# Performance work log

Hardware: AMD Instinct MI355X
Metric: run time of the kernel (lower is better)

Reference implementation:

```python
import jax, jax.numpy as jnp
import numpy as np

KEY_DIM = 32
NUM_HEADS = 8
ATTN_RATIO = 2
D = ATTN_RATIO * KEY_DIM          # 64, per-head value dim
DH = D * NUM_HEADS                # 512
NH_KD = KEY_DIM * NUM_HEADS       # 256
H_QKV = DH + 2 * NH_KD            # 1024
DIM = 512
IMG = 1024                        # img_shape (32x32)
S = 32                            # sqrt(IMG)
ATT = 1044                        # att_shape = N
B = 16
EPS = 1e-5


def hardswish(x):
    return x * jnp.clip(x + 3.0, 0.0, 6.0) / 6.0


def setup_inputs() -> dict:
    key = jax.random.key(0)
    ks = jax.random.split(key, 8)
    x = jax.random.normal(ks[0], (B, ATT, DIM), dtype=jnp.float32)
    qkv_w = jax.random.normal(ks[1], (H_QKV, DIM), dtype=jnp.float32) * 0.02
    bn_gamma = jnp.ones((H_QKV,), dtype=jnp.float32)
    bn_beta = jnp.zeros((H_QKV,), dtype=jnp.float32)
    bn_mean = jax.random.normal(ks[2], (H_QKV,), dtype=jnp.float32) * 0.01
    bn_var = jax.random.uniform(ks[3], (H_QKV,), minval=0.5, maxval=1.5, dtype=jnp.float32)
    conv_w = jax.random.normal(ks[4], (DH, 1, 3, 3), dtype=jnp.float32) * 0.1  # depthwise
    conv_b = jnp.zeros((DH,), dtype=jnp.float32)
    proj_w = jax.random.normal(ks[5], (IMG, ATT), dtype=jnp.float32) * 0.02
    proj_b = jnp.zeros((IMG,), dtype=jnp.float32)
    out_w = jax.random.normal(ks[6], (DIM, DH), dtype=jnp.float32) * 0.02
    out_b = jnp.zeros((DIM,), dtype=jnp.float32)
    return {"x": x, "qkv_w": qkv_w, "bn_gamma": bn_gamma, "bn_beta": bn_beta,
            "bn_mean": bn_mean, "bn_var": bn_var, "conv_w": conv_w, "conv_b": conv_b,
            "proj_w": proj_w, "proj_b": proj_b, "out_w": out_w, "out_b": out_b}


def reference(x, qkv_w, bn_gamma, bn_beta, bn_mean, bn_var,
              conv_w, conv_b, proj_w, proj_b, out_w, out_b):
    Bb, N, C = x.shape
    # Linear_BN: linear (no bias) + BatchNorm1d (eval, running stats)
    qkv = jnp.einsum('bnc,hc->bnh', x, qkv_w)
    qkv = (qkv - bn_mean) * (bn_gamma * jax.lax.rsqrt(bn_var + EPS)) + bn_beta
    qkv = qkv.reshape(Bb, N, NUM_HEADS, 2 * KEY_DIM + D)
    q = qkv[..., :KEY_DIM].transpose(0, 2, 1, 3)                 # (B,H,N,kd)
    k = qkv[..., KEY_DIM:2 * KEY_DIM].transpose(0, 2, 1, 3)      # (B,H,N,kd)
    v = qkv[..., 2 * KEY_DIM:].transpose(0, 2, 1, 3)             # (B,H,N,d)
    # parallel depthwise conv branch: raw reshape (B,H,IMG,d) -> (B,DH,S,S), as in torch
    v0 = v[:, :, :IMG, :].reshape(Bb, DH, S, S)
    vc = jax.lax.conv_general_dilated(
        hardswish(v0), conv_w, window_strides=(1, 1), padding='SAME',
        dimension_numbers=('NCHW', 'OIHW', 'NCHW'), feature_group_count=DH)
    vc = (vc + conv_b[None, :, None, None]).reshape(Bb, DH, IMG)  # (B,DH,IMG)
    # attention
    attn = jax.nn.softmax(jnp.einsum('bhnk,bhmk->bhnm', q, k) * (KEY_DIM ** -0.5), axis=-1)
    o = jnp.einsum('bhnm,bhmd->bhnd', attn, v)                   # (B,H,N,d)
    # torch: (attn@v).transpose(1,2).reshape(B,-1,N) -> raw flatten of (B,N,H,d) into (B,DH,N)
    o = o.transpose(0, 2, 1, 3).reshape(Bb, DH, N)
    xo = jnp.einsum('bdn,mn->bdm', o, proj_w) + proj_b + vc       # (B,DH,IMG)
    out = jnp.einsum('bmd,cd->bmc', xo.transpose(0, 2, 1), out_w) + out_b  # (B,IMG,DIM)
    return out
```

## Files before the change

kernel.cpp:

```cpp
#include <hip/hip_runtime.h>
#include <hip/hip_fp16.h>

typedef _Float16 f16;
typedef _Float16 f16x8 __attribute__((ext_vector_type(8)));
typedef _Float16 f16x4 __attribute__((ext_vector_type(4)));
typedef float    f32x4 __attribute__((ext_vector_type(4)));
typedef float    f32x16 __attribute__((ext_vector_type(16)));

#define DEV __device__ __forceinline__

DEV int imin(int a, int b) { return a < b ? a : b; }

#if defined(__has_builtin)
#  if __has_builtin(__builtin_amdgcn_exp2f)
#    define EXP2(x) __builtin_amdgcn_exp2f(x)
#  else
#    define EXP2(x) __expf((x) * 0.6931471805599453f)
#  endif
#else
#  define EXP2(x) __expf((x) * 0.6931471805599453f)
#endif

#define QSCALE (0.17677669529663687f * 1.4426950408889634f)


constexpr size_t OFF_XH   = 0;
constexpr size_t OFF_WQ   = 17104896;
constexpr size_t OFF_PW   = 18153472;
constexpr size_t OFF_OW   = 20316160;
constexpr size_t OFF_BNA  = 20840448;
constexpr size_t OFF_BNB  = 20844544;
constexpr size_t OFF_QB   = 20848640;
constexpr size_t OFF_KB   = 30285824;
constexpr size_t OFF_VT   = 39198720;
constexpr size_t OFF_OPAD = 57024512;
constexpr size_t OFF_VCT  = 74326016;
constexpr size_t OFF_XOT  = 91103232;

DEV f32x16 zero16() {
  f32x16 z;
  #pragma unroll
  for (int i = 0; i < 16; ++i) z[i] = 0.f;
  return z;
}

DEV unsigned pk2(float a, float b) {
  auto h = __builtin_amdgcn_cvt_pkrtz(a, b);
  union { decltype(h) x; unsigned u; } t;
  t.x = h;
  return t.u;
}

DEV void plswap(unsigned &a, unsigned &b) {
  asm("v_permlane32_swap_b32 %0, %1" : "+v"(a), "+v"(b));
}

union W4 { unsigned w[4]; f16x8 v; };

DEV void pack_block(const float p[16], f16x8 &a0, f16x8 &a1) {
  unsigned w0 = pk2(p[0], p[1]),   w1 = pk2(p[2], p[3]);
  unsigned w2 = pk2(p[4], p[5]),   w3 = pk2(p[6], p[7]);
  unsigned w4 = pk2(p[8], p[9]),   w5 = pk2(p[10], p[11]);
  unsigned w6 = pk2(p[12], p[13]), w7 = pk2(p[14], p[15]);
  plswap(w0, w2); plswap(w1, w3);
  plswap(w4, w6); plswap(w5, w7);
  W4 u; u.w[0] = w0; u.w[1] = w1; u.w[2] = w2; u.w[3] = w3; a0 = u.v;
  W4 v; v.w[0] = w4; v.w[1] = w5; v.w[2] = w6; v.w[3] = w7; a1 = v.v;
}

__global__ __launch_bounds__(256) void prep_kernel(
    const float* __restrict__ x, const float* __restrict__ qkv_w,
    const float* __restrict__ bn_g, const float* __restrict__ bn_b,
    const float* __restrict__ bn_m, const float* __restrict__ bn_v,
    const float* __restrict__ proj_w, const float* __restrict__ out_w,
    f16* __restrict__ x_h, f16* __restrict__ wq_h, f16* __restrict__ pw_h,
    f16* __restrict__ ow_h, float* __restrict__ bn_a, float* __restrict__ bn_sh,
    f16* __restrict__ qb, f16* __restrict__ kb, f16* __restrict__ vt,
    f16* __restrict__ opad)
{
  long tid = (long)blockIdx.x * blockDim.x + threadIdx.x;
  long gsz = (long)gridDim.x * blockDim.x;

  for (long i = tid; i < 2138112; i += gsz) {
    float4 f = ((const float4*)x)[i];
    f16x4 o = {(f16)f.x, (f16)f.y, (f16)f.z, (f16)f.w};
    ((f16x4*)x_h)[i] = o;
  }
  for (long i = tid; i < 524288; i += gsz) wq_h[i] = (f16)qkv_w[i];
  for (long i = tid; i < 1081344; i += gsz) {
    long m = i / 1056, nn = i - m * 1056;
    pw_h[i] = (nn < 1044) ? (f16)proj_w[m * 1044 + nn] : (f16)0.f;
  }
  for (long i = tid; i < 262144; i += gsz) ow_h[i] = (f16)out_w[i];
  for (long i = tid; i < 1024; i += gsz) {
    float a = bn_g[i] * rsqrtf(bn_v[i] + 1e-5f);
    bn_a[i] = a;
    bn_sh[i] = bn_b[i] - bn_m[i] * a;
  }
  for (long i = tid; i < 13824; i += gsz) {
    int bh = (int)(i / 108);
    int nn = 1044 + (int)(i - (long)bh * 108);
    f16* q = qb + ((long)bh * 1152 + nn) * 32;
    for (int j = 0; j < 32; ++j) q[j] = (f16)0.f;
  }
  for (long i = tid; i < 5632; i += gsz) {
    int bh = (int)(i / 44);
    int nn = 1044 + (int)(i - (long)bh * 44);
    f16* k = kb + ((long)bh * 1088 + nn) * 32;
    for (int j = 0; j < 32; ++j) k[j] = (f16)0.f;
  }
  for (long i = tid; i < 8192; i += gsz) {
    f16* v = vt + i * 1088 + 1044;
    for (int j = 0; j < 44; ++j) v[j] = (f16)0.f;
  }
  for (long i = tid; i < 8192; i += gsz) {
    f16* o = opad + i * 1056 + 1044;
    for (int j = 0; j < 12; ++j) o[j] = (f16)0.f;
  }
}

DEV void gemm_core(const f16* __restrict__ A, const f16* __restrict__ B,
                   int lda, int ldb, int kIters, int rowClampA, int rowClampB,
                   f16* As, f16* Bs, f32x4 acc[4][4])
{
  const int t = threadIdx.x;
  const int wave = t >> 6, lane = t & 63;
  const int wr = wave >> 1, wc = wave & 1;
  const int r0 = t >> 2, seg = t & 3;
  const int fr = lane & 15, fg = lane >> 4;
  const int ra0 = imin(r0, rowClampA);
  const int ra1 = imin(r0 + 64, rowClampA);
  const int rb0 = imin(r0, rowClampB);
  const int rb1 = imin(r0 + 64, rowClampB);

  const f16* pa0 = A + (long)ra0 * lda + seg * 8;
  const f16* pa1 = A + (long)ra1 * lda + seg * 8;
  const f16* pb0 = B + (long)rb0 * ldb + seg * 8;
  const f16* pb1 = B + (long)rb1 * ldb + seg * 8;

  f16x8 a0, a1, b0, b1;
  a0 = *(const f16x8*)(pa0);
  a1 = *(const f16x8*)(pa1);
  b0 = *(const f16x8*)(pb0);
  b1 = *(const f16x8*)(pb1);

  #pragma unroll 1
  for (int kt = 0; kt < kIters; ++kt) {
    __syncthreads();
    *(f16x8*)(As + r0 * 40 + seg * 8) = a0;
    *(f16x8*)(As + (r0 + 64) * 40 + seg * 8) = a1;
    *(f16x8*)(Bs + r0 * 40 + seg * 8) = b0;
    *(f16x8*)(Bs + (r0 + 64) * 40 + seg * 8) = b1;
    __syncthreads();
    if (kt + 1 < kIters) {
      const int kb = (kt + 1) * 32;
      a0 = *(const f16x8*)(pa0 + kb);
      a1 = *(const f16x8*)(pa1 + kb);
      b0 = *(const f16x8*)(pb0 + kb);
      b1 = *(const f16x8*)(pb1 + kb);
    }
    f16x8 af[4], bf[4];
    #pragma unroll
    for (int m = 0; m < 4; ++m)
      af[m] = *(const f16x8*)(As + (wr * 64 + m * 16 + fr) * 40 + fg * 8);
    #pragma unroll
    for (int n = 0; n < 4; ++n)
      bf[n] = *(const f16x8*)(Bs + (wc * 64 + n * 16 + fr) * 40 + fg * 8);
    #pragma unroll
    for (int m = 0; m < 4; ++m)
      #pragma unroll
      for (int n = 0; n < 4; ++n)
        acc[m][n] = __builtin_amdgcn_mfma_f32_16x16x32_f16(af[m], bf[n], acc[m][n], 0, 0, 0);
  }
}

__global__ __launch_bounds__(256) void qkv_gemm(
    const f16* __restrict__ x_h, const f16* __restrict__ wq,
    const float* __restrict__ bn_a, const float* __restrict__ bn_sh,
    f16* __restrict__ qb, f16* __restrict__ kb, f16* __restrict__ vt)
{
  __shared__ f16 As[128 * 40];
  __shared__ f16 Bs[128 * 40];
  const int id = blockIdx.x + blockIdx.y * 8;
  const int lin = (id & 7) * 131 + (id >> 3);
  const int row0 = (lin & 7) * 128;
  const int col0 = (lin >> 3) * 128;
  f32x4 acc[4][4];
  #pragma unroll
  for (int m = 0; m < 4; ++m)
    #pragma unroll
    for (int n = 0; n < 4; ++n) acc[m][n] = (f32x4){0.f, 0.f, 0.f, 0.f};
  gemm_core(wq + (long)row0 * 512, x_h + (long)col0 * 512, 512, 512, 16,
            1 << 30, 16703 - col0, As, Bs, acc);
  const int lane = threadIdx.x & 63, wave = threadIdx.x >> 6;
  const int wr = wave >> 1, wc = wave & 1, fr = lane & 15, fg = lane >> 4;
  #pragma unroll
  for (int m = 0; m < 4; ++m) {
    const int chBase = row0 + wr * 64 + m * 16 + fg * 4;
    const float4 ba4 = *(const float4*)(bn_a + chBase);
    const float4 bs4 = *(const float4*)(bn_sh + chBase);
    const int hh = chBase >> 7, r = chBase & 127;
    #pragma unroll
    for (int n = 0; n < 4; ++n) {
      int tok = col0 + wc * 64 + n * 16 + fr;
      if (tok < 16704) {
        int bi = tok / 1044;
        int ni = tok - bi * 1044;
        long bh = (long)(bi * 8 + hh);
        float v0 = acc[m][n][0] * ba4.x + bs4.x;
        float v1 = acc[m][n][1] * ba4.y + bs4.y;
        float v2 = acc[m][n][2] * ba4.z + bs4.z;
        float v3 = acc[m][n][3] * ba4.w + bs4.w;
        if (r < 32) {
          f16x4 pk = {(f16)(v0 * QSCALE), (f16)(v1 * QSCALE),
                      (f16)(v2 * QSCALE), (f16)(v3 * QSCALE)};
          *(f16x4*)(qb + (bh * 1152 + ni) * 32 + r) = pk;
        } else if (r < 64) {
          f16x4 pk = {(f16)v0, (f16)v1, (f16)v2, (f16)v3};
          *(f16x4*)(kb + (bh * 1088 + ni) * 32 + (r - 32)) = pk;
        } else {
          f16* vp = vt + (bh * 64 + (r - 64)) * 1088 + ni;
          vp[0]        = (f16)v0;
          vp[1088]     = (f16)v1;
          vp[2 * 1088] = (f16)v2;
          vp[3 * 1088] = (f16)v3;
        }
      }
    }
  }
}

__global__ __launch_bounds__(256) void conv_kernel(
    const f16* __restrict__ vt, const float* __restrict__ conv_w,
    const float* __restrict__ conv_b, f16* __restrict__ vcT)
{
  __shared__ f16 img[16][34][36];
  const int b = blockIdx.y, g = blockIdx.x;
  const int c0 = g * 16, h = c0 >> 6, ci0 = c0 & 63;
  const int t = threadIdx.x;
  for (int i = t; i < 16 * 34 * 36; i += 256) ((f16*)img)[i] = (f16)0.f;
  __syncthreads();
  const int d = t >> 2, seg = t & 3;
  const f16* src = vt + ((long)(b * 8 + h) * 64 + d) * 1088 + ci0 * 16 + seg * 64;
  const int dhib = d >> 5;
  const int s2 = d & 31;
  #pragma unroll
  for (int j = 0; j < 8; ++j) {
    f16x8 vv = *(const f16x8*)(src + j * 8);
    #pragma unroll
    for (int e = 0; e < 8; ++e) {
      int local = seg * 64 + j * 8 + e;
      int cl = local >> 4, rr = local & 15;
      float xv = (float)vv[e];
      float hs = xv * fminf(fmaxf(xv + 3.f, 0.f), 6.f) * (1.f / 6.f);
      img[cl][1 + rr * 2 + dhib][1 + s2] = (f16)hs;
    }
  }
  __syncthreads();
  const int cl = t & 15, pg = t >> 4;
  const int c = c0 + cl;
  float w[9];
  #pragma unroll
  for (int i = 0; i < 9; ++i) w[i] = conv_w[c * 9 + i];
  const float bias = conv_b[c];
  for (int i = 0; i < 64; ++i) {
    int p = pg + i * 16;
    int s1 = p >> 5, ss2 = p & 31;
    float a = bias;
    #pragma unroll
    for (int di = 0; di < 3; ++di)
      #pragma unroll
      for (int dj = 0; dj < 3; ++dj)
        a += w[di * 3 + dj] * (float)img[cl][s1 + di][ss2 + dj];
    vcT[((long)b * 1024 + p) * 512 + c] = (f16)a;
  }
}

__global__ __launch_bounds__(256, 4) void attn_kernel(
    const f16* __restrict__ qb, const f16* __restrict__ kb,
    const f16* __restrict__ vt, f16* __restrict__ opad)
{
  __shared__ f16 kls[2][4 * 32 * 8];
  __shared__ f16 vls[2][4 * 64 * 8];
  __shared__ float l_sh[4][32];

  const int id = blockIdx.x + blockIdx.y * 9;
  const int xcd = id & 7, sl = id >> 3;
  const int bh = xcd * 16 + sl / 9, qblk = sl % 9;
  const int b = bh >> 3, h = bh & 7;
  const int t = threadIdx.x;
  const int wave = t >> 6, lane = t & 63;
  const int lq = lane & 31, hi = lane >> 5;
  const int q0 = qblk * 128 + wave * 32;

  const f16* qb_ = qb + (long)bh * 1152 * 32;
  const f16* kb_ = kb + (long)bh * 1088 * 32;
  const f16* vt_ = vt + (long)bh * 64 * 1088;

  const f16x8 qf0 = *(const f16x8*)(qb_ + (long)(q0 + lq) * 32 + hi * 8);
  const f16x8 qf1 = *(const f16x8*)(qb_ + (long)(q0 + lq) * 32 + 16 + hi * 8);

  const int sk_k = t >> 3, sk_s8 = t & 7;
  const int sk_seg = sk_s8 >> 1, sk_half = sk_s8 & 1;
  const int sv_d = t >> 2, sv_p = t & 3;
  const int wkoff = (sk_seg * 32 + ((sk_k + sk_seg) & 31)) * 16 + sk_half * 8;
  const int wvoff = (sv_p * 64 + ((sv_d + sv_p) & 63)) * 16;
  int koff[2], voff[2][2];
  #pragma unroll
  for (int ss = 0; ss < 2; ++ss) {
    int ss2 = 2 * ss + hi;
    koff[ss] = (ss2 * 32 + ((lq + ss2) & 31)) * 16;
  }
  #pragma unroll
  for (int nd = 0; nd < 2; ++nd)
    #pragma unroll
    for (int ks = 0; ks < 2; ++ks) {
      int kk4 = 2 * ks + hi;
      voff[nd][ks] = (kk4 * 64 + ((nd * 32 + lq + kk4) & 63)) * 16;
    }

  f16x4 stk;
  f16x8 stv;
  auto load_tile = [&](int kt) {
    stk = *(const f16x4*)(kb_ + (long)(kt * 32 + sk_k) * 32 + sk_s8 * 4);
    stv = *(const f16x8*)(vt_ + (long)sv_d * 1088 + kt * 32 + sv_p * 8);
  };
  auto write_tile = [&](int buf) {
    *(f16x4*)((char*)kls[buf] + wkoff) = stk;
    *(f16x8*)((char*)vls[buf] + wvoff) = stv;
  };

  f32x16 o0 = zero16(), o1 = zero16();
  float lsum = 0.f;

  load_tile(0);
  write_tile(0);
  __syncthreads();

  int cur = 0;
  #pragma unroll 1
  for (int kt = 0; kt < 33; ++kt) {
    if (kt < 32) load_tile(kt + 1);
    const char* kcur = (const char*)kls[cur];
    const char* vcur = (const char*)vls[cur];
    f16x8 kf0 = *(const f16x8*)(kcur + koff[0]);
    f16x8 kf1 = *(const f16x8*)(kcur + koff[1]);
    f32x16 s = zero16();
    s = __builtin_amdgcn_mfma_f32_32x32x16_f16(kf0, qf0, s, 0, 0, 0);
    s = __builtin_amdgcn_mfma_f32_32x32x16_f16(kf1, qf1, s, 0, 0, 0);
    float p[16];
    #pragma unroll
    for (int r = 0; r < 16; ++r) p[r] = EXP2(s[r]);
    if (kt == 32) {
      #pragma unroll
      for (int r = 0; r < 16; ++r) {
        int cr = (r & 3) + 8 * (r >> 2) + 4 * hi;
        p[r] = (cr < 20) ? p[r] : 0.f;
      }
    }
    float t8[8];
    #pragma unroll
    for (int r = 0; r < 8; ++r) t8[r] = p[r] + p[r + 8];
    lsum += ((t8[0] + t8[1]) + (t8[2] + t8[3])) + ((t8[4] + t8[5]) + (t8[6] + t8[7]));
    f16x8 pa0, pa1;
    pack_block(p, pa0, pa1);
    __builtin_amdgcn_s_setprio(1);
    {
      f16x8 vf00 = *(const f16x8*)(vcur + voff[0][0]);
      f16x8 vf10 = *(const f16x8*)(vcur + voff[1][0]);
      o0 = __builtin_amdgcn_mfma_f32_32x32x16_f16(pa0, vf00, o0, 0, 0, 0);
      o1 = __builtin_amdgcn_mfma_f32_32x32x16_f16(pa0, vf10, o1, 0, 0, 0);
      f16x8 vf01 = *(const f16x8*)(vcur + voff[0][1]);
      f16x8 vf11 = *(const f16x8*)(vcur + voff[1][1]);
      o0 = __builtin_amdgcn_mfma_f32_32x32x16_f16(pa1, vf01, o0, 0, 0, 0);
      o1 = __builtin_amdgcn_mfma_f32_32x32x16_f16(pa1, vf11, o1, 0, 0, 0);
    }
    __builtin_amdgcn_s_setprio(0);
    if (kt < 32) write_tile(cur ^ 1);
    __syncthreads();
    cur ^= 1;
  }

  lsum += __shfl_xor(lsum, 32);
  l_sh[wave][lq] = lsum;
  __syncthreads();
  float invl[16];
  #pragma unroll
  for (int r = 0; r < 16; ++r) {
    int cr = (r & 3) + 8 * (r >> 2) + 4 * hi;
    invl[r] = __builtin_amdgcn_rcpf(l_sh[wave][cr]);
  }
  #pragma unroll
  for (int nd = 0; nd < 2; ++nd) {
    #pragma unroll
    for (int r = 0; r < 16; ++r) {
      int cr = (r & 3) + 8 * (r >> 2) + 4 * hi;
      int q = q0 + cr;
      if (q < 1044) {
        float val = (nd ? o1[r] : o0[r]) * invl[r];
        unsigned flat = (unsigned)q * 512u + (unsigned)h * 64u + (unsigned)(nd * 32 + lq);
        unsigned c = flat / 1044u;
        unsigned np = flat - c * 1044u;
        opad[((long)b * 512 + c) * 1056 + np] = (f16)val;
      }
    }
  }
}

__global__ __launch_bounds__(256) void proj_gemm(
    const f16* __restrict__ pw, const f16* __restrict__ opad,
    const float* __restrict__ proj_b, const f16* __restrict__ vcT,
    f16* __restrict__ xoT)
{
  __shared__ f16 As[128 * 40];
  __shared__ f16 Bs[128 * 40];
  const int id = blockIdx.x + blockIdx.y * 4 + blockIdx.z * 32;
  const int lin = (id & 7) * 64 + (id >> 3);
  const int b = lin >> 5;
  const int rc = lin & 31;
  const int row0 = (rc >> 2) * 128;
  const int col0 = (rc & 3) * 128;
  f32x4 acc[4][4];
  #pragma unroll
  for (int m = 0; m < 4; ++m)
    #pragma unroll
    for (int n = 0; n < 4; ++n) acc[m][n] = (f32x4){0.f, 0.f, 0.f, 0.f};
  gemm_core(pw + (long)row0 * 1056, opad + ((long)b * 512 + col0) * 1056,
            1056, 1056, 33, 1 << 30, 1 << 30, As, Bs, acc);
  const int lane = threadIdx.x & 63, wave = threadIdx.x >> 6;
  const int wr = wave >> 1, wc = wave & 1, fr = lane & 15, fg = lane >> 4;
  #pragma unroll
  for (int m = 0; m < 4; ++m) {
    #pragma unroll
    for (int rr = 0; rr < 4; ++rr) {
      int mi = row0 + wr * 64 + m * 16 + fg * 4 + rr;
      float pb = proj_b[mi];
      #pragma unroll
      for (int n = 0; n < 4; ++n) {
        int c = col0 + wc * 64 + n * 16 + fr;
        long idx = ((long)b * 1024 + mi) * 512 + c;
        xoT[idx] = (f16)(acc[m][n][rr] + pb + (float)vcT[idx]);
      }
    }
  }
}

__global__ __launch_bounds__(256) void out_gemm(
    const f16* __restrict__ xoT, const f16* __restrict__ ow,
    const float* __restrict__ out_b, float* __restrict__ out)
{
  __shared__ f16 As[128 * 40];
  __shared__ f16 Bs[128 * 40];
  const int id = blockIdx.x + blockIdx.y * 4 + blockIdx.z * 32;
  const int lin = (id & 7) * 64 + (id >> 3);
  const int b = lin >> 5;
  const int rc = lin & 31;
  const int row0 = (rc >> 2) * 128;
  const int col0 = (rc & 3) * 128;
  f32x4 acc[4][4];
  #pragma unroll
  for (int m = 0; m < 4; ++m)
    #pragma unroll
    for (int n = 0; n < 4; ++n) acc[m][n] = (f32x4){0.f, 0.f, 0.f, 0.f};
  gemm_core(xoT + ((long)b * 1024 + row0) * 512, ow + (long)col0 * 512,
            512, 512, 16, 1 << 30, 1 << 30, As, Bs, acc);
  const int lane = threadIdx.x & 63, wave = threadIdx.x >> 6;
  const int wr = wave >> 1, wc = wave & 1, fr = lane & 15, fg = lane >> 4;
  float ob[4];
  #pragma unroll
  for (int n = 0; n < 4; ++n) ob[n] = out_b[col0 + wc * 64 + n * 16 + fr];
  #pragma unroll
  for (int m = 0; m < 4; ++m) {
    #pragma unroll
    for (int rr = 0; rr < 4; ++rr) {
      int mi = row0 + wr * 64 + m * 16 + fg * 4 + rr;
      #pragma unroll
      for (int n = 0; n < 4; ++n) {
        int co = col0 + wc * 64 + n * 16 + fr;
        out[((long)b * 1024 + mi) * 512 + co] = acc[m][n][rr] + ob[n];
      }
    }
  }
}

extern "C" void kernel_launch(void* const* d_in, const int* in_sizes, int n_in,
                              void* d_out, int out_size, void* d_ws, size_t ws_size,
                              hipStream_t stream) {
  const float* x      = (const float*)d_in[0];
  const float* qkv_w  = (const float*)d_in[1];
  const float* bn_g   = (const float*)d_in[2];
  const float* bn_b   = (const float*)d_in[3];
  const float* bn_m   = (const float*)d_in[4];
  const float* bn_v   = (const float*)d_in[5];
  const float* conv_w = (const float*)d_in[6];
  const float* conv_b = (const float*)d_in[7];
  const float* proj_w = (const float*)d_in[8];
  const float* proj_b = (const float*)d_in[9];
  const float* out_w  = (const float*)d_in[10];
  const float* out_b  = (const float*)d_in[11];
  float* out = (float*)d_out;

  char* ws = (char*)d_ws;
  f16*   x_h   = (f16*)(ws + OFF_XH);
  f16*   wq_h  = (f16*)(ws + OFF_WQ);
  f16*   pw_h  = (f16*)(ws + OFF_PW);
  f16*   ow_h  = (f16*)(ws + OFF_OW);
  float* bn_a  = (float*)(ws + OFF_BNA);
  float* bn_sh = (float*)(ws + OFF_BNB);
  f16*   qb    = (f16*)(ws + OFF_QB);
  f16*   kb    = (f16*)(ws + OFF_KB);
  f16*   vt    = (f16*)(ws + OFF_VT);
  f16*   opad  = (f16*)(ws + OFF_OPAD);
  f16*   vcT   = (f16*)(ws + OFF_VCT);
  f16*   xoT   = (f16*)(ws + OFF_XOT);

  prep_kernel<<<1024, 256, 0, stream>>>(x, qkv_w, bn_g, bn_b, bn_m, bn_v,
                                        proj_w, out_w, x_h, wq_h, pw_h, ow_h,
                                        bn_a, bn_sh, qb, kb, vt, opad);
  qkv_gemm<<<dim3(8, 131), 256, 0, stream>>>(x_h, wq_h, bn_a, bn_sh, qb, kb, vt);
  conv_kernel<<<dim3(32, 16), 256, 0, stream>>>(vt, conv_w, conv_b, vcT);
  attn_kernel<<<dim3(9, 128), 256, 0, stream>>>(qb, kb, vt, opad);
  proj_gemm<<<dim3(4, 8, 16), 256, 0, stream>>>(pw_h, opad, proj_b, vcT, xoT);
  out_gemm<<<dim3(4, 8, 16), 256, 0, stream>>>(xoT, ow_h, out_b, out);
}
```

Baseline: 176.0 us.

## Have each attention wave process two 32-row query tiles to reuse K/V fragments

Halves the attention block size to two waves, and each wave now handles 64 query rows as two 32-row sub-tiles sharing the same K and V fragments loaded from LDS. Staging loads are widened so 128 threads still fill the K/V tiles, and the final normalisation reads per-row sums for both sub-tiles. This cuts LDS reads and barrier overhead per unit of MFMA work, at the cost of doubled accumulator registers and fewer waves per block, which may lower occupancy.

```diff
diff --git a/kernel.cpp b/kernel.cpp
--- a/kernel.cpp
+++ b/kernel.cpp
@@ -276,13 +276,13 @@
   }
 }
 
-__global__ __launch_bounds__(256, 4) void attn_kernel(
+__global__ __launch_bounds__(128) void attn_kernel(
     const f16* __restrict__ qb, const f16* __restrict__ kb,
     const f16* __restrict__ vt, f16* __restrict__ opad)
 {
   __shared__ f16 kls[2][4 * 32 * 8];
   __shared__ f16 vls[2][4 * 64 * 8];
-  __shared__ float l_sh[4][32];
+  __shared__ float l_sh[2][64];
 
   const int id = blockIdx.x + blockIdx.y * 9;
   const int xcd = id & 7, sl = id >> 3;
@@ -291,20 +291,23 @@
   const int t = threadIdx.x;
   const int wave = t >> 6, lane = t & 63;
   const int lq = lane & 31, hi = lane >> 5;
-  const int q0 = qblk * 128 + wave * 32;
+  const int q0 = qblk * 128 + wave * 64;
 
   const f16* qb_ = qb + (long)bh * 1152 * 32;
   const f16* kb_ = kb + (long)bh * 1088 * 32;
   const f16* vt_ = vt + (long)bh * 64 * 1088;
 
-  const f16x8 qf0 = *(const f16x8*)(qb_ + (long)(q0 + lq) * 32 + hi * 8);
-  const f16x8 qf1 = *(const f16x8*)(qb_ + (long)(q0 + lq) * 32 + 16 + hi * 8);
-
-  const int sk_k = t >> 3, sk_s8 = t & 7;
-  const int sk_seg = sk_s8 >> 1, sk_half = sk_s8 & 1;
-  const int sv_d = t >> 2, sv_p = t & 3;
-  const int wkoff = (sk_seg * 32 + ((sk_k + sk_seg) & 31)) * 16 + sk_half * 8;
-  const int wvoff = (sv_p * 64 + ((sv_d + sv_p) & 63)) * 16;
+  const f16x8 qfA0 = *(const f16x8*)(qb_ + (long)(q0 + lq) * 32 + hi * 8);
+  const f16x8 qfA1 = *(const f16x8*)(qb_ + (long)(q0 + lq) * 32 + 16 + hi * 8);
+  const f16x8 qfB0 = *(const f16x8*)(qb_ + (long)(q0 + 32 + lq) * 32 + hi * 8);
+  const f16x8 qfB1 = *(const f16x8*)(qb_ + (long)(q0 + 32 + lq) * 32 + 16 + hi * 8);
+
+  const int sk_k = t >> 2, sk_s = t & 3;
+  const int sv_d = t >> 1, sv_p = t & 1;
+  const int c0v = 2 * sv_p, c1v = c0v + 1;
+  const int wkoff = (sk_s * 32 + ((sk_k + sk_s) & 31)) * 16;
+  const int wvoff0 = (c0v * 64 + ((sv_d + c0v) & 63)) * 16;
+  const int wvoff1 = (c1v * 64 + ((sv_d + c1v) & 63)) * 16;
   int koff[2], voff[2][2];
   #pragma unroll
   for (int ss = 0; ss < 2; ++ss) {
@@ -319,19 +322,20 @@
       voff[nd][ks] = (kk4 * 64 + ((nd * 32 + lq + kk4) & 63)) * 16;
     }
 
-  f16x4 stk;
-  f16x8 stv;
+  f16x8 stk, stv0, stv1;
   auto load_tile = [&](int kt) {
-    stk = *(const f16x4*)(kb_ + (long)(kt * 32 + sk_k) * 32 + sk_s8 * 4);
-    stv = *(const f16x8*)(vt_ + (long)sv_d * 1088 + kt * 32 + sv_p * 8);
+    stk  = *(const f16x8*)(kb_ + (long)(kt * 32 + sk_k) * 32 + sk_s * 8);
+    stv0 = *(const f16x8*)(vt_ + (long)sv_d * 1088 + kt * 32 + sv_p * 16);
+    stv1 = *(const f16x8*)(vt_ + (long)sv_d * 1088 + kt * 32 + sv_p * 16 + 8);
   };
   auto write_tile = [&](int buf) {
-    *(f16x4*)((char*)kls[buf] + wkoff) = stk;
-    *(f16x8*)((char*)vls[buf] + wvoff) = stv;
+    *(f16x8*)((char*)kls[buf] + wkoff)  = stk;
+    *(f16x8*)((char*)vls[buf] + wvoff0) = stv0;
+    *(f16x8*)((char*)vls[buf] + wvoff1) = stv1;
   };
 
-  f32x16 o0 = zero16(), o1 = zero16();
-  float lsum = 0.f;
+  f32x16 oA0 = zero16(), oA1 = zero16(), oB0 = zero16(), oB1 = zero16();
+  float lsumA = 0.f, lsumB = 0.f;
 
   load_tile(0);
   write_tile(0);
@@ -345,35 +349,46 @@
     const char* vcur = (const char*)vls[cur];
     f16x8 kf0 = *(const f16x8*)(kcur + koff[0]);
     f16x8 kf1 = *(const f16x8*)(kcur + koff[1]);
-    f32x16 s = zero16();
-    s = __builtin_amdgcn_mfma_f32_32x32x16_f16(kf0, qf0, s, 0, 0, 0);
-    s = __builtin_amdgcn_mfma_f32_32x32x16_f16(kf1, qf1, s, 0, 0, 0);
-    float p[16];
-    #pragma unroll
-    for (int r = 0; r < 16; ++r) p[r] = EXP2(s[r]);
+    f32x16 sA = zero16(), sB = zero16();
+    sA = __builtin_amdgcn_mfma_f32_32x32x16_f16(kf0, qfA0, sA, 0, 0, 0);
+    sB = __builtin_amdgcn_mfma_f32_32x32x16_f16(kf0, qfB0, sB, 0, 0, 0);
+    sA = __builtin_amdgcn_mfma_f32_32x32x16_f16(kf1, qfA1, sA, 0, 0, 0);
+    sB = __builtin_amdgcn_mfma_f32_32x32x16_f16(kf1, qfB1, sB, 0, 0, 0);
+    float pA[16], pB[16];
+    #pragma unroll
+    for (int r = 0; r < 16; ++r) { pA[r] = EXP2(sA[r]); pB[r] = EXP2(sB[r]); }
     if (kt == 32) {
       #pragma unroll
       for (int r = 0; r < 16; ++r) {
         int cr = (r & 3) + 8 * (r >> 2) + 4 * hi;
-        p[r] = (cr < 20) ? p[r] : 0.f;
+        pA[r] = (cr < 20) ? pA[r] : 0.f;
+        pB[r] = (cr < 20) ? pB[r] : 0.f;
       }
     }
     float t8[8];
     #pragma unroll
-    for (int r = 0; r < 8; ++r) t8[r] = p[r] + p[r + 8];
-    lsum += ((t8[0] + t8[1]) + (t8[2] + t8[3])) + ((t8[4] + t8[5]) + (t8[6] + t8[7]));
-    f16x8 pa0, pa1;
-    pack_block(p, pa0, pa1);
+    for (int r = 0; r < 8; ++r) t8[r] = pA[r] + pA[r + 8];
+    lsumA += ((t8[0] + t8[1]) + (t8[2] + t8[3])) + ((t8[4] + t8[5]) + (t8[6] + t8[7]));
+    #pragma unroll
+    for (int r = 0; r < 8; ++r) t8[r] = pB[r] + pB[r + 8];
+    lsumB += ((t8[0] + t8[1]) + (t8[2] + t8[3])) + ((t8[4] + t8[5]) + (t8[6] + t8[7]));
+    f16x8 paA0, paA1, paB0, paB1;
+    pack_block(pA, paA0, paA1);
+    pack_block(pB, paB0, paB1);
     __builtin_amdgcn_s_setprio(1);
     {
       f16x8 vf00 = *(const f16x8*)(vcur + voff[0][0]);
       f16x8 vf10 = *(const f16x8*)(vcur + voff[1][0]);
-      o0 = __builtin_amdgcn_mfma_f32_32x32x16_f16(pa0, vf00, o0, 0, 0, 0);
-      o1 = __builtin_amdgcn_mfma_f32_32x32x16_f16(pa0, vf10, o1, 0, 0, 0);
+      oA0 = __builtin_amdgcn_mfma_f32_32x32x16_f16(paA0, vf00, oA0, 0, 0, 0);
+      oB0 = __builtin_amdgcn_mfma_f32_32x32x16_f16(paB0, vf00, oB0, 0, 0, 0);
+      oA1 = __builtin_amdgcn_mfma_f32_32x32x16_f16(paA0, vf10, oA1, 0, 0, 0);
+      oB1 = __builtin_amdgcn_mfma_f32_32x32x16_f16(paB0, vf10, oB1, 0, 0, 0);
       f16x8 vf01 = *(const f16x8*)(vcur + voff[0][1]);
       f16x8 vf11 = *(const f16x8*)(vcur + voff[1][1]);
-      o0 = __builtin_amdgcn_mfma_f32_32x32x16_f16(pa1, vf01, o0, 0, 0, 0);
-      o1 = __builtin_amdgcn_mfma_f32_32x32x16_f16(pa1, vf11, o1, 0, 0, 0);
+      oA0 = __builtin_amdgcn_mfma_f32_32x32x16_f16(paA1, vf01, oA0, 0, 0, 0);
+      oB0 = __builtin_amdgcn_mfma_f32_32x32x16_f16(paB1, vf01, oB0, 0, 0, 0);
+      oA1 = __builtin_amdgcn_mfma_f32_32x32x16_f16(paA1, vf11, oA1, 0, 0, 0);
+      oB1 = __builtin_amdgcn_mfma_f32_32x32x16_f16(paB1, vf11, oB1, 0, 0, 0);
     }
     __builtin_amdgcn_s_setprio(0);
     if (kt < 32) write_tile(cur ^ 1);
@@ -381,27 +396,28 @@
     cur ^= 1;
   }
 
-  lsum += __shfl_xor(lsum, 32);
-  l_sh[wave][lq] = lsum;
+  lsumA += __shfl_xor(lsumA, 32);
+  lsumB += __shfl_xor(lsumB, 32);
+  l_sh[wave][lq] = lsumA;
+  l_sh[wave][32 + lq] = lsumB;
   __syncthreads();
-  float invl[16];
-  #pragma unroll
-  for (int r = 0; r < 16; ++r) {
-    int cr = (r & 3) + 8 * (r >> 2) + 4 * hi;
-    invl[r] = __builtin_amdgcn_rcpf(l_sh[wave][cr]);
-  }
-  #pragma unroll
-  for (int nd = 0; nd < 2; ++nd) {
-    #pragma unroll
-    for (int r = 0; r < 16; ++r) {
-      int cr = (r & 3) + 8 * (r >> 2) + 4 * hi;
-      int q = q0 + cr;
-      if (q < 1044) {
-        float val = (nd ? o1[r] : o0[r]) * invl[r];
-        unsigned flat = (unsigned)q * 512u + (unsigned)h * 64u + (unsigned)(nd * 32 + lq);
-        unsigned c = flat / 1044u;
-        unsigned np = flat - c * 1044u;
-        opad[((long)b * 512 + c) * 1056 + np] = (f16)val;
+  #pragma unroll
+  for (int g = 0; g < 2; ++g) {
+    #pragma unroll
+    for (int nd = 0; nd < 2; ++nd) {
+      #pragma unroll
+      for (int r = 0; r < 16; ++r) {
+        int cr = (r & 3) + 8 * (r >> 2) + 4 * hi;
+        int q = q0 + g * 32 + cr;
+        if (q < 1044) {
+          float inv = __builtin_amdgcn_rcpf(l_sh[wave][g * 32 + cr]);
+          float o = g ? (nd ? oB1[r] : oB0[r]) : (nd ? oA1[r] : oA0[r]);
+          float val = o * inv;
+          unsigned flat = (unsigned)q * 512u + (unsigned)h * 64u + (unsigned)(nd * 32 + lq);
+          unsigned c = flat / 1044u;
+          unsigned np = flat - c * 1044u;
+          opad[((long)b * 512 + c) * 1056 + np] = (f16)val;
+        }
       }
     }
   }
@@ -519,7 +535,7 @@
                                         bn_a, bn_sh, qb, kb, vt, opad);
   qkv_gemm<<<dim3(8, 131), 256, 0, stream>>>(x_h, wq_h, bn_a, bn_sh, qb, kb, vt);
   conv_kernel<<<dim3(32, 16), 256, 0, stream>>>(vt, conv_w, conv_b, vcT);
-  attn_kernel<<<dim3(9, 128), 256, 0, stream>>>(qb, kb, vt, opad);
+  attn_kernel<<<dim3(9, 128), 128, 0, stream>>>(qb, kb, vt, opad);
   proj_gemm<<<dim3(4, 8, 16), 256, 0, stream>>>(pw_h, opad, proj_b, vcT, xoT);
   out_gemm<<<dim3(4, 8, 16), 256, 0, stream>>>(xoT, ow_h, out_b, out);
 }
```

Result: slower. 198.7 us (+12.9%).

## Give each wave private K/V LDS staging to drop block barriers in attention

Applied to the files above, without the earlier changes.

The attention kernel now has each wave load its own copy of every K/V tile into a wave-private double-buffered LDS region, so the per-iteration __syncthreads barriers can be removed. This also drops the occupancy hint from launch bounds. The aim is to stop waves stalling on each other at every key tile. In exchange each wave issues four times the global loads and LDS writes, and LDS use per block grows fourfold, which may reduce occupancy. Correctness also now depends on wave-level ordering of LDS reads and writes with no explicit wave barrier.

```diff
diff --git a/kernel.cpp b/kernel.cpp
--- a/kernel.cpp
+++ b/kernel.cpp
@@ -276,12 +276,12 @@
   }
 }
 
-__global__ __launch_bounds__(256, 4) void attn_kernel(
+__global__ __launch_bounds__(256) void attn_kernel(
     const f16* __restrict__ qb, const f16* __restrict__ kb,
     const f16* __restrict__ vt, f16* __restrict__ opad)
 {
-  __shared__ f16 kls[2][4 * 32 * 8];
-  __shared__ f16 vls[2][4 * 64 * 8];
+  __shared__ f16 kls[4][2][4 * 32 * 8];
+  __shared__ f16 vls[4][2][4 * 64 * 8];
   __shared__ float l_sh[4][32];
 
   const int id = blockIdx.x + blockIdx.y * 9;
@@ -300,11 +300,15 @@
   const f16x8 qf0 = *(const f16x8*)(qb_ + (long)(q0 + lq) * 32 + hi * 8);
   const f16x8 qf1 = *(const f16x8*)(qb_ + (long)(q0 + lq) * 32 + 16 + hi * 8);
 
-  const int sk_k = t >> 3, sk_s8 = t & 7;
-  const int sk_seg = sk_s8 >> 1, sk_half = sk_s8 & 1;
-  const int sv_d = t >> 2, sv_p = t & 3;
-  const int wkoff = (sk_seg * 32 + ((sk_k + sk_seg) & 31)) * 16 + sk_half * 8;
-  const int wvoff = (sv_p * 64 + ((sv_d + sv_p) & 63)) * 16;
+  const int rk = lane >> 1;
+  const int ckb = (lane & 1) * 2;
+  const int kwo0 = (ckb * 32 + ((rk + ckb) & 31)) * 16;
+  const int kwo1 = ((ckb + 1) * 32 + ((rk + ckb + 1) & 31)) * 16;
+  const int dv = lane >> 2, cv = lane & 3;
+  int vwo[4];
+  #pragma unroll
+  for (int p = 0; p < 4; ++p)
+    vwo[p] = (cv * 64 + ((p * 16 + dv + cv) & 63)) * 16;
   int koff[2], voff[2][2];
   #pragma unroll
   for (int ss = 0; ss < 2; ++ss) {
@@ -319,30 +323,41 @@
       voff[nd][ks] = (kk4 * 64 + ((nd * 32 + lq + kk4) & 63)) * 16;
     }
 
-  f16x4 stk;
-  f16x8 stv;
+  f16* kbuf0 = kls[wave][0]; f16* kbuf1 = kls[wave][1];
+  f16* vbuf0 = vls[wave][0]; f16* vbuf1 = vls[wave][1];
+
+  f16x8 stk0, stk1, stv0, stv1, stv2, stv3;
   auto load_tile = [&](int kt) {
-    stk = *(const f16x4*)(kb_ + (long)(kt * 32 + sk_k) * 32 + sk_s8 * 4);
-    stv = *(const f16x8*)(vt_ + (long)sv_d * 1088 + kt * 32 + sv_p * 8);
+    const f16* krow = kb_ + (long)(kt * 32 + rk) * 32 + ckb * 8;
+    stk0 = *(const f16x8*)(krow);
+    stk1 = *(const f16x8*)(krow + 8);
+    const f16* vb = vt_ + (long)dv * 1088 + kt * 32 + cv * 8;
+    stv0 = *(const f16x8*)(vb);
+    stv1 = *(const f16x8*)(vb + 16 * 1088);
+    stv2 = *(const f16x8*)(vb + 32 * 1088);
+    stv3 = *(const f16x8*)(vb + 48 * 1088);
   };
-  auto write_tile = [&](int buf) {
-    *(f16x4*)((char*)kls[buf] + wkoff) = stk;
-    *(f16x8*)((char*)vls[buf] + wvoff) = stv;
+  auto write_tile = [&](f16* kd, f16* vd) {
+    *(f16x8*)((char*)kd + kwo0) = stk0;
+    *(f16x8*)((char*)kd + kwo1) = stk1;
+    *(f16x8*)((char*)vd + vwo[0]) = stv0;
+    *(f16x8*)((char*)vd + vwo[1]) = stv1;
+    *(f16x8*)((char*)vd + vwo[2]) = stv2;
+    *(f16x8*)((char*)vd + vwo[3]) = stv3;
   };
 
   f32x16 o0 = zero16(), o1 = zero16();
   float lsum = 0.f;
 
   load_tile(0);
-  write_tile(0);
-  __syncthreads();
+  write_tile(kbuf0, vbuf0);
 
   int cur = 0;
   #pragma unroll 1
   for (int kt = 0; kt < 33; ++kt) {
     if (kt < 32) load_tile(kt + 1);
-    const char* kcur = (const char*)kls[cur];
-    const char* vcur = (const char*)vls[cur];
+    const char* kcur = (const char*)(cur ? kbuf1 : kbuf0);
+    const char* vcur = (const char*)(cur ? vbuf1 : vbuf0);
     f16x8 kf0 = *(const f16x8*)(kcur + koff[0]);
     f16x8 kf1 = *(const f16x8*)(kcur + koff[1]);
     f32x16 s = zero16();
@@ -376,14 +391,12 @@
       o1 = __builtin_amdgcn_mfma_f32_32x32x16_f16(pa1, vf11, o1, 0, 0, 0);
     }
     __builtin_amdgcn_s_setprio(0);
-    if (kt < 32) write_tile(cur ^ 1);
-    __syncthreads();
+    if (kt < 32) write_tile(cur ? kbuf0 : kbuf1, cur ? vbuf0 : vbuf1);
     cur ^= 1;
   }
 
   lsum += __shfl_xor(lsum, 32);
   l_sh[wave][lq] = lsum;
-  __syncthreads();
   float invl[16];
   #pragma unroll
   for (int r = 0; r < 16; ++r) {
```

Measured after the change: 185.5 us. 1.05x slower.

## Pre-swizzle weight matrices into MFMA fragment order and load them directly from global

Applied to the files above, without the earlier changes.

The prep kernel now writes the qkv, proj and out weights in the per-lane MFMA fragment layout, so each wave fetches its operand fragments with one coalesced 16-byte global load per tile. The weight side no longer goes through shared memory, which halves LDS traffic and the LDS footprint in all three GEMMs. The cost is that weight fragments are read from global/L2 on every k-step by each wave pair with no prefetch one iteration ahead, so load latency may be exposed, and the prep kernel's weight conversion gets more complex index math.

```diff
diff --git a/kernel.cpp b/kernel.cpp
--- a/kernel.cpp
+++ b/kernel.cpp
@@ -25,9 +25,9 @@
 
 
 constexpr size_t OFF_XH   = 0;
-constexpr size_t OFF_WQ   = 17104896;
-constexpr size_t OFF_PW   = 18153472;
-constexpr size_t OFF_OW   = 20316160;
+constexpr size_t OFF_WQF  = 17104896;
+constexpr size_t OFF_PWF  = 18153472;
+constexpr size_t OFF_OWF  = 20316160;
 constexpr size_t OFF_BNA  = 20840448;
 constexpr size_t OFF_BNB  = 20844544;
 constexpr size_t OFF_QB   = 20848640;
@@ -73,8 +73,8 @@
     const float* __restrict__ bn_g, const float* __restrict__ bn_b,
     const float* __restrict__ bn_m, const float* __restrict__ bn_v,
     const float* __restrict__ proj_w, const float* __restrict__ out_w,
-    f16* __restrict__ x_h, f16* __restrict__ wq_h, f16* __restrict__ pw_h,
-    f16* __restrict__ ow_h, float* __restrict__ bn_a, float* __restrict__ bn_sh,
+    f16* __restrict__ x_h, f16* __restrict__ wqF, f16* __restrict__ pwF,
+    f16* __restrict__ owF, float* __restrict__ bn_a, float* __restrict__ bn_sh,
     f16* __restrict__ qb, f16* __restrict__ kb, f16* __restrict__ vt,
     f16* __restrict__ opad)
 {
@@ -86,12 +86,46 @@
     f16x4 o = {(f16)f.x, (f16)f.y, (f16)f.z, (f16)f.w};
     ((f16x4*)x_h)[i] = o;
   }
-  for (long i = tid; i < 524288; i += gsz) wq_h[i] = (f16)qkv_w[i];
-  for (long i = tid; i < 1081344; i += gsz) {
-    long m = i / 1056, nn = i - m * 1056;
-    pw_h[i] = (nn < 1044) ? (f16)proj_w[m * 1044 + nn] : (f16)0.f;
-  }
-  for (long i = tid; i < 262144; i += gsz) ow_h[i] = (f16)out_w[i];
+  for (long i = tid; i < 65536; i += gsz) {
+    int lane = (int)(i & 63);
+    int f = (int)(i >> 6);
+    int m = f & 3, g = (f >> 2) & 1, kt = (f >> 3) & 15, blk = f >> 7;
+    int ch = blk * 128 + g * 64 + m * 16 + (lane & 15);
+    int k  = kt * 32 + (lane >> 4) * 8;
+    const float* src = qkv_w + (long)ch * 512 + k;
+    f16x8 d;
+    #pragma unroll
+    for (int e = 0; e < 8; ++e) d[e] = (f16)src[e];
+    *(f16x8*)(wqF + i * 8) = d;
+  }
+  for (long i = tid; i < 135168; i += gsz) {
+    int lane = (int)(i & 63);
+    int f = (int)(i >> 6);
+    int m = f & 3, g = (f >> 2) & 1;
+    int rest = f >> 3;
+    int kt = rest % 33, blk = rest / 33;
+    int mrow = blk * 128 + g * 64 + m * 16 + (lane & 15);
+    int k = kt * 32 + (lane >> 4) * 8;
+    f16x8 d;
+    #pragma unroll
+    for (int e = 0; e < 8; ++e) {
+      int kk = k + e;
+      d[e] = (kk < 1044) ? (f16)proj_w[(long)mrow * 1044 + kk] : (f16)0.f;
+    }
+    *(f16x8*)(pwF + i * 8) = d;
+  }
+  for (long i = tid; i < 32768; i += gsz) {
+    int lane = (int)(i & 63);
+    int f = (int)(i >> 6);
+    int n = f & 3, g = (f >> 2) & 1, kt = (f >> 3) & 15, blk = f >> 7;
+    int co = blk * 128 + g * 64 + n * 16 + (lane & 15);
+    int k = kt * 32 + (lane >> 4) * 8;
+    const float* src = out_w + (long)co * 512 + k;
+    f16x8 d;
+    #pragma unroll
+    for (int e = 0; e < 8; ++e) d[e] = (f16)src[e];
+    *(f16x8*)(owF + i * 8) = d;
+  }
   for (long i = tid; i < 1024; i += gsz) {
     float a = bn_g[i] * rsqrtf(bn_v[i] + 1e-5f);
     bn_a[i] = a;
@@ -119,53 +153,86 @@
   }
 }
 
-DEV void gemm_core(const f16* __restrict__ A, const f16* __restrict__ B,
-                   int lda, int ldb, int kIters, int rowClampA, int rowClampB,
-                   f16* As, f16* Bs, f32x4 acc[4][4])
+DEV void gemm_coreA(const f16* __restrict__ AF, const f16* __restrict__ B,
+                    long ldb, int kIters, int rowClampB,
+                    f16* Bs, f32x4 acc[4][4])
 {
   const int t = threadIdx.x;
   const int wave = t >> 6, lane = t & 63;
   const int wr = wave >> 1, wc = wave & 1;
   const int r0 = t >> 2, seg = t & 3;
   const int fr = lane & 15, fg = lane >> 4;
-  const int ra0 = imin(r0, rowClampA);
-  const int ra1 = imin(r0 + 64, rowClampA);
   const int rb0 = imin(r0, rowClampB);
   const int rb1 = imin(r0 + 64, rowClampB);
-
-  const f16* pa0 = A + (long)ra0 * lda + seg * 8;
-  const f16* pa1 = A + (long)ra1 * lda + seg * 8;
   const f16* pb0 = B + (long)rb0 * ldb + seg * 8;
   const f16* pb1 = B + (long)rb1 * ldb + seg * 8;
-
-  f16x8 a0, a1, b0, b1;
-  a0 = *(const f16x8*)(pa0);
-  a1 = *(const f16x8*)(pa1);
-  b0 = *(const f16x8*)(pb0);
-  b1 = *(const f16x8*)(pb1);
+  const f16* afp = AF + (long)(wr * 4) * 512 + (long)lane * 8;
+
+  f16x8 b0 = *(const f16x8*)(pb0);
+  f16x8 b1 = *(const f16x8*)(pb1);
+
+  #pragma unroll 1
+  for (int kt = 0; kt < kIters; ++kt) {
+    __syncthreads();
+    *(f16x8*)(Bs + r0 * 40 + seg * 8) = b0;
+    *(f16x8*)(Bs + (r0 + 64) * 40 + seg * 8) = b1;
+    __syncthreads();
+    f16x8 af[4];
+    #pragma unroll
+    for (int m = 0; m < 4; ++m)
+      af[m] = *(const f16x8*)(afp + (long)(kt * 8 + m) * 512);
+    if (kt + 1 < kIters) {
+      const int kb = (kt + 1) * 32;
+      b0 = *(const f16x8*)(pb0 + kb);
+      b1 = *(const f16x8*)(pb1 + kb);
+    }
+    f16x8 bf[4];
+    #pragma unroll
+    for (int n = 0; n < 4; ++n)
+      bf[n] = *(const f16x8*)(Bs + (wc * 64 + n * 16 + fr) * 40 + fg * 8);
+    #pragma unroll
+    for (int m = 0; m < 4; ++m)
+      #pragma unroll
+      for (int n = 0; n < 4; ++n)
+        acc[m][n] = __builtin_amdgcn_mfma_f32_16x16x32_f16(af[m], bf[n], acc[m][n], 0, 0, 0);
+  }
+}
+
+DEV void gemm_coreB(const f16* __restrict__ A, const f16* __restrict__ BF,
+                    long lda, int kIters,
+                    f16* As, f32x4 acc[4][4])
+{
+  const int t = threadIdx.x;
+  const int wave = t >> 6, lane = t & 63;
+  const int wr = wave >> 1, wc = wave & 1;
+  const int r0 = t >> 2, seg = t & 3;
+  const int fr = lane & 15, fg = lane >> 4;
+  const f16* pa0 = A + (long)r0 * lda + seg * 8;
+  const f16* pa1 = A + (long)(r0 + 64) * lda + seg * 8;
+  const f16* bfp = BF + (long)(wc * 4) * 512 + (long)lane * 8;
+
+  f16x8 a0 = *(const f16x8*)(pa0);
+  f16x8 a1 = *(const f16x8*)(pa1);
 
   #pragma unroll 1
   for (int kt = 0; kt < kIters; ++kt) {
     __syncthreads();
     *(f16x8*)(As + r0 * 40 + seg * 8) = a0;
     *(f16x8*)(As + (r0 + 64) * 40 + seg * 8) = a1;
-    *(f16x8*)(Bs + r0 * 40 + seg * 8) = b0;
-    *(f16x8*)(Bs + (r0 + 64) * 40 + seg * 8) = b1;
     __syncthreads();
+    f16x8 bf[4];
+    #pragma unroll
+    for (int n = 0; n < 4; ++n)
+      bf[n] = *(const f16x8*)(bfp + (long)(kt * 8 + n) * 512);
     if (kt + 1 < kIters) {
       const int kb = (kt + 1) * 32;
       a0 = *(const f16x8*)(pa0 + kb);
       a1 = *(const f16x8*)(pa1 + kb);
-      b0 = *(const f16x8*)(pb0 + kb);
-      b1 = *(const f16x8*)(pb1 + kb);
-    }
-    f16x8 af[4], bf[4];
+    }
+    f16x8 af[4];
     #pragma unroll
     for (int m = 0; m < 4; ++m)
       af[m] = *(const f16x8*)(As + (wr * 64 + m * 16 + fr) * 40 + fg * 8);
-    #pragma unroll
-    for (int n = 0; n < 4; ++n)
-      bf[n] = *(const f16x8*)(Bs + (wc * 64 + n * 16 + fr) * 40 + fg * 8);
     #pragma unroll
     for (int m = 0; m < 4; ++m)
       #pragma unroll
@@ -175,11 +242,10 @@
 }
 
 __global__ __launch_bounds__(256) void qkv_gemm(
-    const f16* __restrict__ x_h, const f16* __restrict__ wq,
+    const f16* __restrict__ x_h, const f16* __restrict__ wqF,
     const float* __restrict__ bn_a, const float* __restrict__ bn_sh,
     f16* __restrict__ qb, f16* __restrict__ kb, f16* __restrict__ vt)
 {
-  __shared__ f16 As[128 * 40];
   __shared__ f16 Bs[128 * 40];
   const int id = blockIdx.x + blockIdx.y * 8;
   const int lin = (id & 7) * 131 + (id >> 3);
@@ -190,8 +256,8 @@
   for (int m = 0; m < 4; ++m)
     #pragma unroll
     for (int n = 0; n < 4; ++n) acc[m][n] = (f32x4){0.f, 0.f, 0.f, 0.f};
-  gemm_core(wq + (long)row0 * 512, x_h + (long)col0 * 512, 512, 512, 16,
-            1 << 30, 16703 - col0, As, Bs, acc);
+  gemm_coreA(wqF + (long)(lin & 7) * 65536, x_h + (long)col0 * 512,
+             512, 16, 16703 - col0, Bs, acc);
   const int lane = threadIdx.x & 63, wave = threadIdx.x >> 6;
   const int wr = wave >> 1, wc = wave & 1, fr = lane & 15, fg = lane >> 4;
   #pragma unroll
@@ -408,11 +474,10 @@
 }
 
 __global__ __launch_bounds__(256) void proj_gemm(
-    const f16* __restrict__ pw, const f16* __restrict__ opad,
+    const f16* __restrict__ pwF, const f16* __restrict__ opad,
     const float* __restrict__ proj_b, const f16* __restrict__ vcT,
     f16* __restrict__ xoT)
 {
-  __shared__ f16 As[128 * 40];
   __shared__ f16 Bs[128 * 40];
   const int id = blockIdx.x + blockIdx.y * 4 + blockIdx.z * 32;
   const int lin = (id & 7) * 64 + (id >> 3);
@@ -425,8 +490,8 @@
   for (int m = 0; m < 4; ++m)
     #pragma unroll
     for (int n = 0; n < 4; ++n) acc[m][n] = (f32x4){0.f, 0.f, 0.f, 0.f};
-  gemm_core(pw + (long)row0 * 1056, opad + ((long)b * 512 + col0) * 1056,
-            1056, 1056, 33, 1 << 30, 1 << 30, As, Bs, acc);
+  gemm_coreA(pwF + (long)(rc >> 2) * 135168, opad + ((long)b * 512 + col0) * 1056,
+             1056, 33, 1 << 30, Bs, acc);
   const int lane = threadIdx.x & 63, wave = threadIdx.x >> 6;
   const int wr = wave >> 1, wc = wave & 1, fr = lane & 15, fg = lane >> 4;
   #pragma unroll
@@ -446,11 +511,10 @@
 }
 
 __global__ __launch_bounds__(256) void out_gemm(
-    const f16* __restrict__ xoT, const f16* __restrict__ ow,
+    const f16* __restrict__ xoT, const f16* __restrict__ owF,
     const float* __restrict__ out_b, float* __restrict__ out)
 {
   __shared__ f16 As[128 * 40];
-  __shared__ f16 Bs[128 * 40];
   const int id = blockIdx.x + blockIdx.y * 4 + blockIdx.z * 32;
   const int lin = (id & 7) * 64 + (id >> 3);
   const int b = lin >> 5;
@@ -462,8 +526,8 @@
   for (int m = 0; m < 4; ++m)
     #pragma unroll
     for (int n = 0; n < 4; ++n) acc[m][n] = (f32x4){0.f, 0.f, 0.f, 0.f};
-  gemm_core(xoT + ((long)b * 1024 + row0) * 512, ow + (long)col0 * 512,
-            512, 512, 16, 1 << 30, 1 << 30, As, Bs, acc);
+  gemm_coreB(xoT + ((long)b * 1024 + row0) * 512, owF + (long)(rc & 3) * 65536,
+             512, 16, As, acc);
   const int lane = threadIdx.x & 63, wave = threadIdx.x >> 6;
   const int wr = wave >> 1, wc = wave & 1, fr = lane & 15, fg = lane >> 4;
   float ob[4];
@@ -502,9 +566,9 @@
 
   char* ws = (char*)d_ws;
   f16*   x_h   = (f16*)(ws + OFF_XH);
-  f16*   wq_h  = (f16*)(ws + OFF_WQ);
-  f16*   pw_h  = (f16*)(ws + OFF_PW);
-  f16*   ow_h  = (f16*)(ws + OFF_OW);
+  f16*   wqF   = (f16*)(ws + OFF_WQF);
+  f16*   pwF   = (f16*)(ws + OFF_PWF);
+  f16*   owF   = (f16*)(ws + OFF_OWF);
   float* bn_a  = (float*)(ws + OFF_BNA);
   float* bn_sh = (float*)(ws + OFF_BNB);
   f16*   qb    = (f16*)(ws + OFF_QB);
@@ -515,11 +579,11 @@
   f16*   xoT   = (f16*)(ws + OFF_XOT);
 
   prep_kernel<<<1024, 256, 0, stream>>>(x, qkv_w, bn_g, bn_b, bn_m, bn_v,
-                                        proj_w, out_w, x_h, wq_h, pw_h, ow_h,
+                                        proj_w, out_w, x_h, wqF, pwF, owF,
                                         bn_a, bn_sh, qb, kb, vt, opad);
-  qkv_gemm<<<dim3(8, 131), 256, 0, stream>>>(x_h, wq_h, bn_a, bn_sh, qb, kb, vt);
+  qkv_gemm<<<dim3(8, 131), 256, 0, stream>>>(x_h, wqF, bn_a, bn_sh, qb, kb, vt);
   conv_kernel<<<dim3(32, 16), 256, 0, stream>>>(vt, conv_w, conv_b, vcT);
   attn_kernel<<<dim3(9, 128), 256, 0, stream>>>(qb, kb, vt, opad);
-  proj_gemm<<<dim3(4, 8, 16), 256, 0, stream>>>(pw_h, opad, proj_b, vcT, xoT);
-  out_gemm<<<dim3(4, 8, 16), 256, 0, stream>>>(xoT, ow_h, out_b, out);
-}
+  proj_gemm<<<dim3(4, 8, 16), 256, 0, stream>>>(pwF, opad, proj_b, vcT, xoT);
+  out_gemm<<<dim3(4, 8, 16), 256, 0, stream>>>(xoT, owF, out_b, out);
+}
```

New measurement: 184.1 us. 4.6% more time.
